# Kernel optimization log

Hardware: AMD Instinct MI355X
Metric: run time of the kernel (lower is better)

Reference implementation:

```python
import jax, jax.numpy as jnp
import numpy as np

N_NODES = 100000
N_EDGES = 1600000
IN_C, HID_C, OUT_C = 128, 256, 47


def setup_inputs() -> dict:
    key = jax.random.key(0)
    ks = jax.random.split(key, 8)
    x = jax.random.normal(ks[0], (N_NODES, IN_C), dtype=jnp.float32)
    edge_index = jax.random.randint(ks[1], (2, N_EDGES), 0, N_NODES, dtype=jnp.int64)

    def glorot(k, fan_in, fan_out):
        s = 1.0 / np.sqrt(fan_in)
        return jax.random.uniform(k, (fan_in, fan_out), jnp.float32, -s, s)

    W1_l = glorot(ks[2], IN_C, HID_C)
    b1 = jnp.zeros((HID_C,), jnp.float32)
    W1_r = glorot(ks[3], IN_C, HID_C)
    W2_l = glorot(ks[4], HID_C, OUT_C)
    b2 = jnp.zeros((OUT_C,), jnp.float32)
    W2_r = glorot(ks[5], HID_C, OUT_C)
    return {"x": x, "edge_index": edge_index,
            "W1_l": W1_l, "b1": b1, "W1_r": W1_r,
            "W2_l": W2_l, "b2": b2, "W2_r": W2_r}


def _sage_conv(x, src, dst, W_l, b, W_r, num_nodes):
    # mean aggregation of source-node features onto destination nodes
    msg_sum = jax.ops.segment_sum(x[src], dst, num_segments=num_nodes)  # [N, C]
    cnt = jax.ops.segment_sum(jnp.ones((src.shape[0], 1), x.dtype), dst,
                              num_segments=num_nodes)                   # [N, 1]
    mean = msg_sum / jnp.maximum(cnt, 1.0)
    # out = lin_l(mean) + lin_r(x_root); lin_l carries the bias (PyG default)
    return mean @ W_l + b + x @ W_r


def reference(x, edge_index, W1_l, b1, W1_r, W2_l, b2, W2_r):
    num_nodes = x.shape[0]
    src, dst = edge_index[0], edge_index[1]
    h = _sage_conv(x, src, dst, W1_l, b1, W1_r, num_nodes)
    h = jax.nn.relu(h)  # dropout is identity in eval mode
    out = _sage_conv(h, src, dst, W2_l, b2, W2_r, num_nodes)
    return jax.nn.log_softmax(out, axis=-1)
```

## Files before the change

### kernel.cpp

```cpp
#include <hip/hip_runtime.h>
#include <hip/hip_bf16.h>

constexpr int IN_C  = 128;
constexpr int HID_C = 256;
constexpr int OUT_C = 47;

typedef __attribute__((ext_vector_type(8))) short bf16x8;
typedef __attribute__((ext_vector_type(4))) float f32x4;

static __device__ __forceinline__ unsigned short f2bf(float v) {
  __hip_bfloat16 hb = __float2bfloat16(v);
  return *(unsigned short*)&hb;
}
static __device__ __forceinline__ float bf2f(unsigned short u) {
  return __uint_as_float((unsigned)u << 16);
}


__global__ void count_edges(const int* __restrict__ dst, int* __restrict__ cnt, int E) {
  int e = blockIdx.x * blockDim.x + threadIdx.x;
  if (e < E) atomicAdd(&cnt[dst[e]], 1);
}

__global__ __launch_bounds__(256) void scan_partials(const int* __restrict__ cnt,
                                                     int* __restrict__ part, int N) {
  const int i0 = blockIdx.x * 1024 + threadIdx.x * 4;
  int s = 0;
  if (i0 + 3 < N) {
    const int4 v = *(const int4*)&cnt[i0];
    s = v.x + v.y + v.z + v.w;
  } else {
    for (int k = 0; k < 4; ++k) { const int i = i0 + k; if (i < N) s += cnt[i]; }
  }
  #pragma unroll
  for (int o = 32; o > 0; o >>= 1) s += __shfl_xor(s, o, 64);
  __shared__ int ws[4];
  if ((threadIdx.x & 63) == 0) ws[threadIdx.x >> 6] = s;
  __syncthreads();
  if (threadIdx.x == 0) part[blockIdx.x] = ws[0] + ws[1] + ws[2] + ws[3];
}

__global__ __launch_bounds__(1024) void scan_roots(int* __restrict__ part,
                                                   int* __restrict__ off, int nb, int N) {
  __shared__ int tmp[1024];
  const int t = threadIdx.x;
  const int v = (t < nb) ? part[t] : 0;
  tmp[t] = v;
  __syncthreads();
  for (int d = 1; d < 1024; d <<= 1) {
    const int u = (t >= d) ? tmp[t - d] : 0;
    __syncthreads();
    tmp[t] += u;
    __syncthreads();
  }
  if (t < nb) part[t] = tmp[t] - v;
  if (t == 1023) off[N] = tmp[1023];
}

__global__ __launch_bounds__(256) void scan_write(const int* __restrict__ cnt,
                                                  const int* __restrict__ part,
                                                  int* __restrict__ off, int N) {
  const int b = blockIdx.x;
  const int i0 = b * 1024 + threadIdx.x * 4;
  int4 v = make_int4(0, 0, 0, 0);
  if (i0 + 3 < N) v = *(const int4*)&cnt[i0];
  else {
    int* p = (int*)&v;
    for (int k = 0; k < 4; ++k) { const int i = i0 + k; if (i < N) p[k] = cnt[i]; }
  }
  const int tsum = v.x + v.y + v.z + v.w;
  const int lane = threadIdx.x & 63;
  int incl = tsum;
  #pragma unroll
  for (int o = 1; o < 64; o <<= 1) {
    const int u = __shfl_up(incl, o, 64);
    if (lane >= o) incl += u;
  }
  __shared__ int wsum[4];
  const int wv = threadIdx.x >> 6;
  if (lane == 63) wsum[wv] = incl;
  __syncthreads();
  int wbase = 0;
  for (int w = 0; w < wv; ++w) wbase += wsum[w];
  const int tbase = part[b] + wbase + incl - tsum;
  int4 ov;
  ov.x = tbase;
  ov.y = tbase + v.x;
  ov.z = tbase + v.x + v.y;
  ov.w = tbase + v.x + v.y + v.z;
  if (i0 + 3 < N) *(int4*)&off[i0] = ov;
  else {
    int* p = (int*)&ov;
    for (int k = 0; k < 4; ++k) { const int i = i0 + k; if (i < N) off[i] = p[k]; }
  }
}

__global__ void fill_csr(const int* __restrict__ src, const int* __restrict__ dst,
                         const int* __restrict__ off, int* __restrict__ cursor,
                         int* __restrict__ csr, int E) {
  int e = blockIdx.x * blockDim.x + threadIdx.x;
  if (e < E) {
    int d = dst[e];
    int p = atomicAdd(&cursor[d], 1);
    csr[off[d] + p] = src[e];
  }
}

__global__ void f32_to_bf16(const float* __restrict__ in, unsigned short* __restrict__ out, int n4) {
  int i = blockIdx.x * blockDim.x + threadIdx.x;
  if (i < n4) {
    float4 v = *(const float4*)&in[i * 4];
    ushort4 o;
    o.x = f2bf(v.x); o.y = f2bf(v.y); o.z = f2bf(v.z); o.w = f2bf(v.w);
    *(ushort4*)&out[i * 4] = o;
  }
}

__global__ __launch_bounds__(256) void agg1(const unsigned short* __restrict__ xb,
                                            const int* __restrict__ off,
                                            const int* __restrict__ csr,
                                            unsigned short* __restrict__ meanb, int N) {
  const int wid  = (blockIdx.x * blockDim.x + threadIdx.x) >> 6;
  const int lane = threadIdx.x & 63;
  if (wid >= N) return;
  const unsigned* xw = (const unsigned*)xb;
  const int s0 = off[wid], s1 = off[wid + 1];
  float a0 = 0.f, a1 = 0.f, b0 = 0.f, b1 = 0.f;
  float c0 = 0.f, c1 = 0.f, d0 = 0.f, d1 = 0.f;
  for (int base = s0; base < s1; base += 64) {
    const int cnt = min(64, s1 - base);
    const int idx = (lane < cnt) ? csr[base + lane] : 0;
    int e = 0;
    for (; e + 4 <= cnt; e += 4) {
      const int sA = __shfl(idx, e, 64),     sB = __shfl(idx, e + 1, 64);
      const int sC = __shfl(idx, e + 2, 64), sD = __shfl(idx, e + 3, 64);
      const unsigned uA = xw[(size_t)sA * 64 + lane];
      const unsigned uB = xw[(size_t)sB * 64 + lane];
      const unsigned uC = xw[(size_t)sC * 64 + lane];
      const unsigned uD = xw[(size_t)sD * 64 + lane];
      a0 += __uint_as_float(uA << 16); a1 += __uint_as_float(uA & 0xffff0000u);
      b0 += __uint_as_float(uB << 16); b1 += __uint_as_float(uB & 0xffff0000u);
      c0 += __uint_as_float(uC << 16); c1 += __uint_as_float(uC & 0xffff0000u);
      d0 += __uint_as_float(uD << 16); d1 += __uint_as_float(uD & 0xffff0000u);
    }
    for (; e < cnt; ++e) {
      const int sA = __shfl(idx, e, 64);
      const unsigned uA = xw[(size_t)sA * 64 + lane];
      a0 += __uint_as_float(uA << 16); a1 += __uint_as_float(uA & 0xffff0000u);
    }
  }
  const float r0 = (a0 + b0) + (c0 + d0);
  const float r1 = (a1 + b1) + (c1 + d1);
  const int deg = s1 - s0;
  const float inv = (deg > 0) ? 1.0f / (float)deg : 0.0f;
  const unsigned lo = f2bf(r0 * inv), hi = f2bf(r1 * inv);
  ((unsigned*)meanb)[(size_t)wid * 64 + lane] = lo | (hi << 16);
}

__global__ void build_w1cat_t(const float* __restrict__ Wl, const float* __restrict__ Wr,
                              unsigned short* __restrict__ BT) {
  int idx = blockIdx.x * blockDim.x + threadIdx.x;
  if (idx < 256 * 256) {
    int j = idx >> 8, k = idx & 255;
    float v = (k < 128) ? Wl[k * 256 + j] : Wr[(k - 128) * 256 + j];
    BT[idx] = f2bf(v);
  }
}
__global__ void build_w2cat_t(const float* __restrict__ Wl, const float* __restrict__ Wr,
                              unsigned short* __restrict__ BT) {
  int idx = blockIdx.x * blockDim.x + threadIdx.x;
  if (idx < 128 * 256) {
    int j = idx >> 8, k = idx & 255;
    float v = 0.f;
    if (j < OUT_C)           v = Wl[k * OUT_C + j];
    else if (j < 2 * OUT_C)  v = Wr[k * OUT_C + (j - OUT_C)];
    BT[idx] = f2bf(v);
  }
}

template<int MODE>
__global__ __launch_bounds__(256) void gemm_mfma(const unsigned short* __restrict__ A0,
                                                 const unsigned short* __restrict__ A1,
                                                 const unsigned short* __restrict__ BT,
                                                 const float* __restrict__ bias,
                                                 unsigned short* __restrict__ Out,
                                                 int M) {
  constexpr int ONC = (MODE == 0) ? 256 : 128;
  __shared__ unsigned short Asl[128 * 64];
  __shared__ unsigned short Bsl[128 * 64];
  const int tid  = threadIdx.x;
  const int wid  = tid >> 6, lane = tid & 63;
  const int wm   = wid >> 1, wn = wid & 1;
  const int r0   = blockIdx.x * 128;
  const int c0   = blockIdx.y * 128;

  f32x4 acc[4][4];
  #pragma unroll
  for (int m = 0; m < 4; ++m)
    #pragma unroll
    for (int n = 0; n < 4; ++n)
      #pragma unroll
      for (int j = 0; j < 4; ++j) acc[m][n][j] = 0.f;

  const int srow = lane >> 3;
  const int cs   = (lane & 7) ^ srow;
  const int fr   = lane & 15;
  const int klo  = (lane >> 4) * 16;
  const int swz  = (fr & 7) << 4;

  #pragma unroll 1
  for (int kb = 0; kb < 4; ++kb) {
    const unsigned short* Ap;
    int acol, ak;
    if (MODE == 0) { Ap = (kb < 2) ? A0 : A1; acol = (kb & 1) * 64; ak = 128; }
    else           { Ap = A0;                 acol = kb * 64;       ak = 256; }
    #pragma unroll
    for (int i = 0; i < 4; ++i) {
      const int rl = wid * 32 + i * 8 + srow;
      int gr = r0 + rl; if (gr > M - 1) gr = M - 1;
      const unsigned short* gsa = Ap + (size_t)gr * ak + acol + cs * 8;
      __builtin_amdgcn_global_load_lds(
          (const __attribute__((address_space(1))) unsigned int*)gsa,
          (__attribute__((address_space(3))) unsigned int*)&Asl[(wid * 32 + i * 8) * 64],
          16, 0, 0);
      const unsigned short* gsb = BT + (size_t)(c0 + rl) * 256 + kb * 64 + cs * 8;
      __builtin_amdgcn_global_load_lds(
          (const __attribute__((address_space(1))) unsigned int*)gsb,
          (__attribute__((address_space(3))) unsigned int*)&Bsl[(wid * 32 + i * 8) * 64],
          16, 0, 0);
    }
    asm volatile("s_waitcnt vmcnt(0)");
    __syncthreads();
    #pragma unroll
    for (int ks = 0; ks < 2; ++ks) {
      bf16x8 af[4], bfv[4];
      #pragma unroll
      for (int m = 0; m < 4; ++m) {
        const int ro = (wm * 64 + m * 16 + fr) * 128 + ((ks * 64 + klo) ^ swz);
        af[m] = *(const bf16x8*)((const char*)Asl + ro);
      }
      #pragma unroll
      for (int n = 0; n < 4; ++n) {
        const int ro = (wn * 64 + n * 16 + fr) * 128 + ((ks * 64 + klo) ^ swz);
        bfv[n] = *(const bf16x8*)((const char*)Bsl + ro);
      }
      #pragma unroll
      for (int m = 0; m < 4; ++m)
        #pragma unroll
        for (int n = 0; n < 4; ++n)
          acc[m][n] = __builtin_amdgcn_mfma_f32_16x16x32_bf16(af[m], bfv[n], acc[m][n], 0, 0, 0);
    }
    __syncthreads();
  }

  const int orow0 = r0 + wm * 64 + (lane >> 4) * 4;
  const int ocol0 = c0 + wn * 64 + (lane & 15);
  #pragma unroll
  for (int m = 0; m < 4; ++m) {
    #pragma unroll
    for (int n = 0; n < 4; ++n) {
      const int col = ocol0 + n * 16;
      const float badd = (MODE == 0) ? bias[col] : 0.f;
      #pragma unroll
      for (int j = 0; j < 4; ++j) {
        const int row = orow0 + m * 16 + j;
        if (row < M) {
          float v = acc[m][n][j] + badd;
          if (MODE == 0) v = fmaxf(v, 0.f);
          Out[(size_t)row * ONC + col] = f2bf(v);
        }
      }
    }
  }
}

__global__ __launch_bounds__(256) void final_kernel(const unsigned short* __restrict__ Ob,
                                                    const int* __restrict__ off,
                                                    const int* __restrict__ csr,
                                                    const float* __restrict__ b2,
                                                    float* __restrict__ out, int N) {
  const int wid  = (blockIdx.x * blockDim.x + threadIdx.x) >> 6;
  const int lane = threadIdx.x & 63;
  if (wid >= N) return;
  const int s0 = off[wid], s1 = off[wid + 1];
  const bool act = lane < OUT_C;
  const int cl = act ? lane : 0;
  float t0 = 0.f, t1 = 0.f, t2 = 0.f, t3 = 0.f;
  for (int base = s0; base < s1; base += 64) {
    const int cnt = min(64, s1 - base);
    const int idx = (lane < cnt) ? csr[base + lane] : 0;
    int e = 0;
    for (; e + 4 <= cnt; e += 4) {
      const int sA = __shfl(idx, e, 64),     sB = __shfl(idx, e + 1, 64);
      const int sC = __shfl(idx, e + 2, 64), sD = __shfl(idx, e + 3, 64);
      if (act) {
        t0 += bf2f(Ob[(size_t)sA * 128 + lane]);
        t1 += bf2f(Ob[(size_t)sB * 128 + lane]);
        t2 += bf2f(Ob[(size_t)sC * 128 + lane]);
        t3 += bf2f(Ob[(size_t)sD * 128 + lane]);
      }
    }
    for (; e < cnt; ++e) {
      const int sA = __shfl(idx, e, 64);
      if (act) t0 += bf2f(Ob[(size_t)sA * 128 + lane]);
    }
  }
  const float sum = (t0 + t1) + (t2 + t3);
  const int deg = s1 - s0;
  const float inv = (deg > 0) ? 1.0f / (float)deg : 0.0f;
  float v = sum * inv + b2[cl] + bf2f(Ob[(size_t)wid * 128 + OUT_C + cl]);
  if (!act) v = -INFINITY;
  float m = v;
  #pragma unroll
  for (int o = 32; o > 0; o >>= 1) m = fmaxf(m, __shfl_xor(m, o, 64));
  float ex = act ? expf(v - m) : 0.f;
  float s = ex;
  #pragma unroll
  for (int o = 32; o > 0; o >>= 1) s += __shfl_xor(s, o, 64);
  if (act) out[(size_t)wid * OUT_C + lane] = v - m - logf(s);
}


extern "C" void kernel_launch(void* const* d_in, const int* in_sizes, int n_in,
                              void* d_out, int out_size, void* d_ws, size_t ws_size,
                              hipStream_t stream) {
  const float* x   = (const float*)d_in[0];
  const int*   ei  = (const int*)d_in[1];
  const float* W1l = (const float*)d_in[2];
  const float* b1  = (const float*)d_in[3];
  const float* W1r = (const float*)d_in[4];
  const float* W2l = (const float*)d_in[5];
  const float* b2  = (const float*)d_in[6];
  const float* W2r = (const float*)d_in[7];
  float* out = (float*)d_out;

  const int N = in_sizes[0] / IN_C;
  const int E = in_sizes[1] / 2;
  const int* src = ei;
  const int* dst = ei + E;

  char* base = (char*)d_ws;
  size_t o = 0;
  auto take = [&](size_t bytes) -> char* {
    char* p = base + o;
    o = (o + bytes + 255) & ~(size_t)255;
    return p;
  };
  int* cnt    = (int*)take((size_t)N * 4);
  int* cursor = (int*)take((size_t)N * 4);
  const size_t zero_bytes = o;
  int* off    = (int*)take((size_t)(N + 1) * 4);
  int* part   = (int*)take((size_t)1024 * 4);
  int* csr    = (int*)take((size_t)E * 4);
  unsigned short* xb    = (unsigned short*)take((size_t)N * IN_C * 2);
  unsigned short* meanb = (unsigned short*)take((size_t)N * IN_C * 2);
  unsigned short* h     = (unsigned short*)take((size_t)N * HID_C * 2);
  unsigned short* W1T   = (unsigned short*)take((size_t)256 * 256 * 2);
  unsigned short* W2T   = (unsigned short*)take((size_t)128 * 256 * 2);
  unsigned short* Ocat  = meanb;
  (void)ws_size; (void)n_in; (void)out_size;

  hipMemsetAsync(base, 0, zero_bytes, stream);

  const int tb = 256;
  const int nb = (N + 1023) / 1024;
  count_edges<<<(E + tb - 1) / tb, tb, 0, stream>>>(dst, cnt, E);
  scan_partials<<<nb, 256, 0, stream>>>(cnt, part, N);
  scan_roots<<<1, 1024, 0, stream>>>(part, off, nb, N);
  scan_write<<<nb, 256, 0, stream>>>(cnt, part, off, N);
  fill_csr<<<(E + tb - 1) / tb, tb, 0, stream>>>(src, dst, off, cursor, csr, E);

  const int n4 = N * IN_C / 4;
  f32_to_bf16<<<(n4 + tb - 1) / tb, tb, 0, stream>>>(x, xb, n4);
  build_w1cat_t<<<256, 256, 0, stream>>>(W1l, W1r, W1T);
  build_w2cat_t<<<128, 256, 0, stream>>>(W2l, W2r, W2T);

  agg1<<<(N + 3) / 4, 256, 0, stream>>>(xb, off, csr, meanb, N);

  const int mb = (N + 127) / 128;
  gemm_mfma<0><<<dim3(mb, 2), 256, 0, stream>>>(meanb, xb, W1T, b1, h, N);
  gemm_mfma<1><<<dim3(mb, 1), 256, 0, stream>>>(h, nullptr, W2T, nullptr, Ocat, N);

  final_kernel<<<(N + 3) / 4, 256, 0, stream>>>(Ocat, off, csr, b2, out, N);
}
```

Measured before the change: 475.7 us.

## Partition CSR fill into destination ranges with grid-stride nontemporal loads

The CSR fill is split into four launches, each handling only edges whose destination falls in a quarter of the node range. This localises the atomic cursor updates and the scattered CSR writes to a smaller working set that may stay in cache. count_edges and the fill kernel now use a fixed 2048-block grid-stride loop with nontemporal loads of the edge arrays. The cost is reading dst four times and adding extra launches.

```diff
diff --git a/kernel.cpp b/kernel.cpp
--- a/kernel.cpp
+++ b/kernel.cpp
@@ -17,9 +17,14 @@
 }
 
 
-__global__ void count_edges(const int* __restrict__ dst, int* __restrict__ cnt, int E) {
+__global__ __launch_bounds__(256) void count_edges(const int* __restrict__ dst,
+                                                   int* __restrict__ cnt, int E) {
   int e = blockIdx.x * blockDim.x + threadIdx.x;
-  if (e < E) atomicAdd(&cnt[dst[e]], 1);
+  const int stride = gridDim.x * blockDim.x;
+  for (; e < E; e += stride) {
+    const int d = __builtin_nontemporal_load(&dst[e]);
+    atomicAdd(&cnt[d], 1);
+  }
 }
 
 __global__ __launch_bounds__(256) void scan_partials(const int* __restrict__ cnt,
@@ -95,14 +100,21 @@
   }
 }
 
-__global__ void fill_csr(const int* __restrict__ src, const int* __restrict__ dst,
-                         const int* __restrict__ off, int* __restrict__ cursor,
-                         int* __restrict__ csr, int E) {
+__global__ __launch_bounds__(256) void fill_csr_range(const int* __restrict__ src,
+                                                      const int* __restrict__ dst,
+                                                      const int* __restrict__ off,
+                                                      int* __restrict__ cursor,
+                                                      int* __restrict__ csr,
+                                                      int E, int lo, int hi) {
   int e = blockIdx.x * blockDim.x + threadIdx.x;
-  if (e < E) {
-    int d = dst[e];
-    int p = atomicAdd(&cursor[d], 1);
-    csr[off[d] + p] = src[e];
+  const int stride = gridDim.x * blockDim.x;
+  for (; e < E; e += stride) {
+    const int d = __builtin_nontemporal_load(&dst[e]);
+    if (d >= lo && d < hi) {
+      const int s = __builtin_nontemporal_load(&src[e]);
+      const int p = atomicAdd(&cursor[d], 1);
+      csr[off[d] + p] = s;
+    }
   }
 }
 
@@ -364,11 +376,18 @@
 
   const int tb = 256;
   const int nb = (N + 1023) / 1024;
-  count_edges<<<(E + tb - 1) / tb, tb, 0, stream>>>(dst, cnt, E);
+  count_edges<<<2048, tb, 0, stream>>>(dst, cnt, E);
   scan_partials<<<nb, 256, 0, stream>>>(cnt, part, N);
   scan_roots<<<1, 1024, 0, stream>>>(part, off, nb, N);
   scan_write<<<nb, 256, 0, stream>>>(cnt, part, off, N);
-  fill_csr<<<(E + tb - 1) / tb, tb, 0, stream>>>(src, dst, off, cursor, csr, E);
+
+  const int P = 4;
+  const int chunk = (N + P - 1) / P;
+  for (int p = 0; p < P; ++p) {
+    const int lo = p * chunk;
+    const int hi = min(N, lo + chunk);
+    fill_csr_range<<<2048, tb, 0, stream>>>(src, dst, off, cursor, csr, E, lo, hi);
+  }
 
   const int n4 = N * IN_C / 4;
   f32_to_bf16<<<(n4 + tb - 1) / tb, tb, 0, stream>>>(x, xb, n4);
```

Result: no change. 475.9 us (+0.0%).
